# Performance work log

Hardware: AMD Instinct MI355X
Metric: run time of the kernel (lower is better)

Reference implementation:

```python
import jax, jax.numpy as jnp
import numpy as np

NUM_JOINTS = 50
FEAT = 3 * NUM_JOINTS  # 150

def _skeleton_bones():
    # Standard 50-joint sign-language skeleton (body + two 21-joint hands).
    body = [(0, 1), (1, 2), (2, 3), (3, 4), (1, 5), (5, 6), (6, 7)]
    def hand(conn_from, wrist):
        bones = [(conn_from, wrist)]
        for f in range(5):  # 5 fingers, chains of 4 joints from the wrist
            base = wrist + 1 + 4 * f
            bones.append((wrist, base))
            for k in range(3):
                bones.append((base + k, base + k + 1))
        return bones
    bones = body + hand(7, 8) + hand(4, 29)  # 49 bones
    bones.append((0, 2))  # pad to 50 bones so 3*num_bones == 150 matches the mask
    return np.asarray(bones, dtype=np.int32)

_BONES = _skeleton_bones()
_BA = jnp.asarray(_BONES[:, 0])  # (50,) bone endpoint a
_BB = jnp.asarray(_BONES[:, 1])  # (50,) bone endpoint b

def get_length_direct(x):
    # x: (B, T, 150) -> lengths (B, T, 50), directs (B, T, 150)
    B, T, _ = x.shape
    joints = x.reshape(B, T, NUM_JOINTS, 3)
    diff = joints[:, :, _BA, :] - joints[:, :, _BB, :]  # (B, T, 50, 3)
    length = jnp.sqrt(jnp.sum(diff * diff, axis=-1, keepdims=True))  # (B, T, 50, 1)
    tiny = jnp.finfo(x.dtype).tiny
    direct = diff / (length + tiny)  # unit directions
    return length[..., 0], direct.reshape(B, T, -1)

def setup_inputs() -> dict:
    key = jax.random.key(0)
    k1, k2 = jax.random.split(key)
    B, T = 64, 4096
    preds = jax.random.normal(k1, (B, T, FEAT), dtype=jnp.float32)
    targets = jax.random.normal(k2, (B, T, FEAT), dtype=jnp.float32)
    return {"preds": preds, "targets": targets}

def reference(preds, targets):
    target_pad = 0.0
    m = (targets != target_pad).astype(preds.dtype)  # (B, T, 150)
    pm = preds * m
    tm = targets * m
    _, pd = get_length_direct(pm)   # (B, T, 150)
    _, td = get_length_direct(tm)
    pd = pd * m  # mask[:, :, :150] == full mask since 3*num_bones == 150
    td = td * m
    # criterion = L1 (mean), criterion_bone = MSE (mean)
    recon = jnp.mean(jnp.abs(pm - tm)) + 0.1 * jnp.mean((pd - td) ** 2)
    return recon
```

## Files before the change

kernel.cpp:

```cpp
#include <hip/hip_runtime.h>

#define NUM_BONES  50
#define FEAT       150
#define FRAMES_PER_BLOCK 32
#define THREADS    256
#define TILE_ELEMS (FRAMES_PER_BLOCK * FEAT)
#define N4         (TILE_ELEMS / 4)
#define NLOAD      5
#define TOTAL_TILES      ((64 * 4096) / FRAMES_PER_BLOCK)
#define GRID_BLOCKS      1024
#define TILES_PER_BLOCK  (TOTAL_TILES / GRID_BLOCKS)

__device__ __constant__ int c_ba[NUM_BONES] = {
    0, 1, 2, 3, 1, 5, 6,
    7, 8, 9, 10, 11, 8, 13, 14, 15, 8, 17, 18, 19,
    8, 21, 22, 23, 8, 25, 26, 27,
    4, 29, 30, 31, 32, 29, 34, 35, 36, 29, 38, 39, 40,
    29, 42, 43, 44, 29, 46, 47, 48,
    0
};
__device__ __constant__ int c_bb[NUM_BONES] = {
    1, 2, 3, 4, 5, 6, 7,
    8, 9, 10, 11, 12, 13, 14, 15, 16, 17, 18, 19, 20,
    21, 22, 23, 24, 25, 26, 27, 28,
    29, 30, 31, 32, 33, 34, 35, 36, 37, 38, 39, 40, 41,
    42, 43, 44, 45, 46, 47, 48, 49,
    2
};

__global__ __launch_bounds__(THREADS)
void loss_main(const float* __restrict__ preds,
               const float* __restrict__ targets,
               double* __restrict__ part0,
               double* __restrict__ part1)
{
    __shared__ float s_pm[TILE_ELEMS];
    __shared__ float s_tm[TILE_ELEMS];

    const int tid = threadIdx.x;
    float l1  = 0.0f;
    float mse = 0.0f;

    const float4* pbase = (const float4*)preds;
    const float4* tbase = (const float4*)targets;
    float4* spm4 = (float4*)s_pm;
    float4* stm4 = (float4*)s_tm;

    int idx[NLOAD];
#pragma unroll
    for (int k = 0; k < NLOAD; ++k) {
        int i = tid + k * THREADS;
        idx[k] = (i < N4) ? i : (N4 - 1);
    }

    float4 pr[NLOAD], tr[NLOAD];
    {
        const long long t0 = (long long)blockIdx.x * N4;
#pragma unroll
        for (int k = 0; k < NLOAD; ++k) {
            pr[k] = pbase[t0 + idx[k]];
            tr[k] = tbase[t0 + idx[k]];
        }
    }

#pragma unroll 1
    for (int j = 0; j < TILES_PER_BLOCK; ++j) {
#pragma unroll
        for (int k = 0; k < NLOAD; ++k) {
            int i = tid + k * THREADS;
            if (i < N4) {
                float4 p = pr[k];
                float4 t = tr[k];
                float4 pm;
                pm.x = (t.x != 0.0f) ? p.x : 0.0f;
                pm.y = (t.y != 0.0f) ? p.y : 0.0f;
                pm.z = (t.z != 0.0f) ? p.z : 0.0f;
                pm.w = (t.w != 0.0f) ? p.w : 0.0f;
                l1 += fabsf(pm.x - t.x) + fabsf(pm.y - t.y)
                    + fabsf(pm.z - t.z) + fabsf(pm.w - t.w);
                spm4[i] = pm;
                stm4[i] = t;
            }
        }
        __syncthreads();

        if (j + 1 < TILES_PER_BLOCK) {
            const long long tn =
                (long long)(blockIdx.x + (j + 1) * GRID_BLOCKS) * N4;
#pragma unroll
            for (int k = 0; k < NLOAD; ++k) {
                pr[k] = pbase[tn + idx[k]];
                tr[k] = tbase[tn + idx[k]];
            }
        }

        const int ntask = FRAMES_PER_BLOCK * NUM_BONES;
#pragma unroll
        for (int k = 0; k < 7; ++k) {
            const int i = tid + k * THREADS;
            if (i < ntask) {
                const int f = i & 31;
                const int b = i >> 5;
                const float* pm = s_pm + f * FEAT;
                const float* tm = s_tm + f * FEAT;
                const int ja = 3 * c_ba[b];
                const int jb = 3 * c_bb[b];

                float dpx = pm[ja]     - pm[jb];
                float dpy = pm[ja + 1] - pm[jb + 1];
                float dpz = pm[ja + 2] - pm[jb + 2];
                float dtx = tm[ja]     - tm[jb];
                float dty = tm[ja + 1] - tm[jb + 1];
                float dtz = tm[ja + 2] - tm[jb + 2];

                float lp2 = dpx * dpx + dpy * dpy + dpz * dpz;
                float lt2 = dtx * dtx + dty * dty + dtz * dtz;
                float ip = (lp2 > 0.0f) ? __builtin_amdgcn_rsqf(lp2) : 0.0f;
                float it = (lt2 > 0.0f) ? __builtin_amdgcn_rsqf(lt2) : 0.0f;

                const int o = 3 * b;
                float e0 = dpx * ip - dtx * it;
                float e1 = dpy * ip - dty * it;
                float e2 = dpz * ip - dtz * it;
                mse += (tm[o]     != 0.0f) ? e0 * e0 : 0.0f;
                mse += (tm[o + 1] != 0.0f) ? e1 * e1 : 0.0f;
                mse += (tm[o + 2] != 0.0f) ? e2 * e2 : 0.0f;
            }
        }
        __syncthreads();
    }

    double v0 = (double)l1;
    double v1 = (double)mse;
    for (int off = 32; off > 0; off >>= 1) {
        v0 += __shfl_down(v0, off, 64);
        v1 += __shfl_down(v1, off, 64);
    }
    __shared__ double s_red0[THREADS / 64];
    __shared__ double s_red1[THREADS / 64];
    const int wave = tid >> 6;
    const int lane = tid & 63;
    if (lane == 0) { s_red0[wave] = v0; s_red1[wave] = v1; }
    __syncthreads();
    if (tid == 0) {
        part0[blockIdx.x] = s_red0[0] + s_red0[1] + s_red0[2] + s_red0[3];
        part1[blockIdx.x] = s_red1[0] + s_red1[1] + s_red1[2] + s_red1[3];
    }
}

__global__ __launch_bounds__(THREADS)
void loss_final(const double* __restrict__ part0,
                const double* __restrict__ part1,
                float* __restrict__ out)
{
    const int tid = threadIdx.x;
    double a = 0.0, b = 0.0;
    for (int i = tid; i < GRID_BLOCKS; i += THREADS) {
        a += part0[i];
        b += part1[i];
    }
    for (int off = 32; off > 0; off >>= 1) {
        a += __shfl_down(a, off, 64);
        b += __shfl_down(b, off, 64);
    }
    __shared__ double s0[THREADS / 64];
    __shared__ double s1[THREADS / 64];
    const int wave = tid >> 6;
    const int lane = tid & 63;
    if (lane == 0) { s0[wave] = a; s1[wave] = b; }
    __syncthreads();
    if (tid == 0) {
        double sa = s0[0] + s0[1] + s0[2] + s0[3];
        double sb = s1[0] + s1[1] + s1[2] + s1[3];
        const double N = 64.0 * 4096.0 * 150.0;
        out[0] = (float)(sa / N + 0.1 * (sb / N));
    }
}

extern "C" void kernel_launch(void* const* d_in, const int* in_sizes, int n_in,
                              void* d_out, int out_size, void* d_ws, size_t ws_size,
                              hipStream_t stream)
{
    (void)in_sizes; (void)n_in; (void)out_size; (void)ws_size;
    const float* preds   = (const float*)d_in[0];
    const float* targets = (const float*)d_in[1];
    double* part0 = (double*)d_ws;
    double* part1 = part0 + GRID_BLOCKS;

    loss_main<<<GRID_BLOCKS, THREADS, 0, stream>>>(preds, targets, part0, part1);
    loss_final<<<1, THREADS, 0, stream>>>(part0, part1, (float*)d_out);
}
```

Measured before the change: 325.6 us.

## Stage tiles via async global-to-LDS loads with double buffering

Replaces the register-staged float4 loads with direct global_load_lds transfers into double-buffered shared memory, using an explicit vmcnt wait and raw barriers so the next tile streams in while the current one is processed. Tiles shrink to 8 frames and the grid doubles to 2048 blocks. Masking and the L1 term move into the per-bone task, which removes the separate mask-and-store pass and precomputes bone offsets once. The hand-written waitcnt counts and LDS offsets are fragile and depend on how the compiler orders the instructions.

```diff
diff --git a/kernel.cpp b/kernel.cpp
--- a/kernel.cpp
+++ b/kernel.cpp
@@ -1,15 +1,16 @@
 #include <hip/hip_runtime.h>
+#include <stdint.h>
 
 #define NUM_BONES  50
 #define FEAT       150
-#define FRAMES_PER_BLOCK 32
+#define FPT        8
 #define THREADS    256
-#define TILE_ELEMS (FRAMES_PER_BLOCK * FEAT)
-#define N4         (TILE_ELEMS / 4)
-#define NLOAD      5
-#define TOTAL_TILES      ((64 * 4096) / FRAMES_PER_BLOCK)
-#define GRID_BLOCKS      1024
-#define TILES_PER_BLOCK  (TOTAL_TILES / GRID_BLOCKS)
+#define TILE_FLOATS (FPT * FEAT)
+#define TOTAL_FRAMES (64 * 4096)
+#define TOTAL_TILES  (TOTAL_FRAMES / FPT)
+#define GRID_BLOCKS  2048
+#define TILES_PER_BLOCK (TOTAL_TILES / GRID_BLOCKS)
+#define NTASK      (FPT * NUM_BONES)
 
 __device__ __constant__ int c_ba[NUM_BONES] = {
     0, 1, 2, 3, 1, 5, 6,
@@ -28,106 +29,118 @@
     2
 };
 
+#define AS1 __attribute__((address_space(1)))
+#define AS3 __attribute__((address_space(3)))
+
+__device__ __forceinline__ void gload16(const float* g, float* l)
+{
+    __builtin_amdgcn_global_load_lds((AS1 unsigned int*)(uintptr_t)g,
+                                     (AS3 unsigned int*)(uintptr_t)l,
+                                     16, 0, 0);
+}
+
+__device__ __forceinline__ void stage_tile(const float* __restrict__ src,
+                                           float* lds, int wv, int ln, int tile)
+{
+    const float* base = src + (size_t)tile * TILE_FLOATS;
+    gload16(base + ((wv * 64 + ln) << 2), lds + wv * 256);
+    if (ln < 11)
+        gload16(base + ((256 + wv * 11 + ln) << 2), lds + 1024 + wv * 44);
+}
+
+__device__ __forceinline__ void bone_task(const float* __restrict__ P,
+                                          const float* __restrict__ T,
+                                          int ja, int jb, int ob,
+                                          float& l1, float& mse)
+{
+    float pax = P[ja], pay = P[ja + 1], paz = P[ja + 2];
+    float pbx = P[jb], pby = P[jb + 1], pbz = P[jb + 2];
+    float tax = T[ja], tay = T[ja + 1], taz = T[ja + 2];
+    float tbx = T[jb], tby = T[jb + 1], tbz = T[jb + 2];
+    float pox = P[ob], poy = P[ob + 1], poz = P[ob + 2];
+    float tox = T[ob], toy = T[ob + 1], toz = T[ob + 2];
+
+    pax = (tax != 0.0f) ? pax : 0.0f;
+    pay = (tay != 0.0f) ? pay : 0.0f;
+    paz = (taz != 0.0f) ? paz : 0.0f;
+    pbx = (tbx != 0.0f) ? pbx : 0.0f;
+    pby = (tby != 0.0f) ? pby : 0.0f;
+    pbz = (tbz != 0.0f) ? pbz : 0.0f;
+    pox = (tox != 0.0f) ? pox : 0.0f;
+    poy = (toy != 0.0f) ? poy : 0.0f;
+    poz = (toz != 0.0f) ? poz : 0.0f;
+
+    l1 += fabsf(pox - tox) + fabsf(poy - toy) + fabsf(poz - toz);
+
+    float dpx = pax - pbx, dpy = pay - pby, dpz = paz - pbz;
+    float dtx = tax - tbx, dty = tay - tby, dtz = taz - tbz;
+    float lp2 = dpx * dpx + dpy * dpy + dpz * dpz;
+    float lt2 = dtx * dtx + dty * dty + dtz * dtz;
+    float ip = (lp2 > 0.0f) ? __builtin_amdgcn_rsqf(lp2) : 0.0f;
+    float it = (lt2 > 0.0f) ? __builtin_amdgcn_rsqf(lt2) : 0.0f;
+    float e0 = dpx * ip - dtx * it;
+    float e1 = dpy * ip - dty * it;
+    float e2 = dpz * ip - dtz * it;
+    mse += (tox != 0.0f) ? e0 * e0 : 0.0f;
+    mse += (toy != 0.0f) ? e1 * e1 : 0.0f;
+    mse += (toz != 0.0f) ? e2 * e2 : 0.0f;
+}
+
 __global__ __launch_bounds__(THREADS)
 void loss_main(const float* __restrict__ preds,
                const float* __restrict__ targets,
                double* __restrict__ part0,
                double* __restrict__ part1)
 {
-    __shared__ float s_pm[TILE_ELEMS];
-    __shared__ float s_tm[TILE_ELEMS];
+    __shared__ float s_p[2][TILE_FLOATS];
+    __shared__ float s_t[2][TILE_FLOATS];
 
     const int tid = threadIdx.x;
-    float l1  = 0.0f;
-    float mse = 0.0f;
-
-    const float4* pbase = (const float4*)preds;
-    const float4* tbase = (const float4*)targets;
-    float4* spm4 = (float4*)s_pm;
-    float4* stm4 = (float4*)s_tm;
-
-    int idx[NLOAD];
-#pragma unroll
-    for (int k = 0; k < NLOAD; ++k) {
-        int i = tid + k * THREADS;
-        idx[k] = (i < N4) ? i : (N4 - 1);
-    }
-
-    float4 pr[NLOAD], tr[NLOAD];
+    const int wv = tid >> 6;
+    const int ln = tid & 63;
+
+    int ja0, jb0, ob0, ja1, jb1, ob1;
     {
-        const long long t0 = (long long)blockIdx.x * N4;
-#pragma unroll
-        for (int k = 0; k < NLOAD; ++k) {
-            pr[k] = pbase[t0 + idx[k]];
-            tr[k] = tbase[t0 + idx[k]];
-        }
-    }
+        int f = tid & 7, b = tid >> 3;
+        ja0 = f * FEAT + 3 * c_ba[b];
+        jb0 = f * FEAT + 3 * c_bb[b];
+        ob0 = f * FEAT + 3 * b;
+        int i1 = tid + THREADS;
+        int ii = (i1 < NTASK) ? i1 : 0;
+        f = ii & 7; b = ii >> 3;
+        ja1 = f * FEAT + 3 * c_ba[b];
+        jb1 = f * FEAT + 3 * c_bb[b];
+        ob1 = f * FEAT + 3 * b;
+    }
+
+    float l1 = 0.0f, mse = 0.0f;
+
+    stage_tile(preds,   s_p[0], wv, ln, (int)blockIdx.x);
+    stage_tile(targets, s_t[0], wv, ln, (int)blockIdx.x);
 
 #pragma unroll 1
     for (int j = 0; j < TILES_PER_BLOCK; ++j) {
-#pragma unroll
-        for (int k = 0; k < NLOAD; ++k) {
-            int i = tid + k * THREADS;
-            if (i < N4) {
-                float4 p = pr[k];
-                float4 t = tr[k];
-                float4 pm;
-                pm.x = (t.x != 0.0f) ? p.x : 0.0f;
-                pm.y = (t.y != 0.0f) ? p.y : 0.0f;
-                pm.z = (t.z != 0.0f) ? p.z : 0.0f;
-                pm.w = (t.w != 0.0f) ? p.w : 0.0f;
-                l1 += fabsf(pm.x - t.x) + fabsf(pm.y - t.y)
-                    + fabsf(pm.z - t.z) + fabsf(pm.w - t.w);
-                spm4[i] = pm;
-                stm4[i] = t;
-            }
+        const int bs = j & 1;
+        if (j + 1 < TILES_PER_BLOCK) {
+            const int tn = (int)blockIdx.x + (j + 1) * GRID_BLOCKS;
+            stage_tile(preds,   s_p[bs ^ 1], wv, ln, tn);
+            stage_tile(targets, s_t[bs ^ 1], wv, ln, tn);
+            asm volatile("s_waitcnt vmcnt(4)" ::: "memory");
+        } else {
+            asm volatile("s_waitcnt vmcnt(0)" ::: "memory");
         }
-        __syncthreads();
-
-        if (j + 1 < TILES_PER_BLOCK) {
-            const long long tn =
-                (long long)(blockIdx.x + (j + 1) * GRID_BLOCKS) * N4;
-#pragma unroll
-            for (int k = 0; k < NLOAD; ++k) {
-                pr[k] = pbase[tn + idx[k]];
-                tr[k] = tbase[tn + idx[k]];
-            }
-        }
-
-        const int ntask = FRAMES_PER_BLOCK * NUM_BONES;
-#pragma unroll
-        for (int k = 0; k < 7; ++k) {
-            const int i = tid + k * THREADS;
-            if (i < ntask) {
-                const int f = i & 31;
-                const int b = i >> 5;
-                const float* pm = s_pm + f * FEAT;
-                const float* tm = s_tm + f * FEAT;
-                const int ja = 3 * c_ba[b];
-                const int jb = 3 * c_bb[b];
-
-                float dpx = pm[ja]     - pm[jb];
-                float dpy = pm[ja + 1] - pm[jb + 1];
-                float dpz = pm[ja + 2] - pm[jb + 2];
-                float dtx = tm[ja]     - tm[jb];
-                float dty = tm[ja + 1] - tm[jb + 1];
-                float dtz = tm[ja + 2] - tm[jb + 2];
-
-                float lp2 = dpx * dpx + dpy * dpy + dpz * dpz;
-                float lt2 = dtx * dtx + dty * dty + dtz * dtz;
-                float ip = (lp2 > 0.0f) ? __builtin_amdgcn_rsqf(lp2) : 0.0f;
-                float it = (lt2 > 0.0f) ? __builtin_amdgcn_rsqf(lt2) : 0.0f;
-
-                const int o = 3 * b;
-                float e0 = dpx * ip - dtx * it;
-                float e1 = dpy * ip - dty * it;
-                float e2 = dpz * ip - dtz * it;
-                mse += (tm[o]     != 0.0f) ? e0 * e0 : 0.0f;
-                mse += (tm[o + 1] != 0.0f) ? e1 * e1 : 0.0f;
-                mse += (tm[o + 2] != 0.0f) ? e2 * e2 : 0.0f;
-            }
-        }
-        __syncthreads();
+        __builtin_amdgcn_sched_barrier(0);
+        __builtin_amdgcn_s_barrier();
+        __builtin_amdgcn_sched_barrier(0);
+
+        const float* P = s_p[bs];
+        const float* T = s_t[bs];
+        bone_task(P, T, ja0, jb0, ob0, l1, mse);
+        if (tid < (NTASK - THREADS))
+            bone_task(P, T, ja1, jb1, ob1, l1, mse);
+
+        __builtin_amdgcn_sched_barrier(0);
+        __builtin_amdgcn_s_barrier();
     }
 
     double v0 = (double)l1;
@@ -138,9 +151,7 @@
     }
     __shared__ double s_red0[THREADS / 64];
     __shared__ double s_red1[THREADS / 64];
-    const int wave = tid >> 6;
-    const int lane = tid & 63;
-    if (lane == 0) { s_red0[wave] = v0; s_red1[wave] = v1; }
+    if (ln == 0) { s_red0[wv] = v0; s_red1[wv] = v1; }
     __syncthreads();
     if (tid == 0) {
         part0[blockIdx.x] = s_red0[0] + s_red0[1] + s_red0[2] + s_red0[3];
```

Measured after the change: 325.1 us. No clear change (-0.2%).
